# Kernel optimization log

Measured on AMD Instinct MI355X. Metric: run time of the kernel, lower is better.

## Reference

```python
import jax, jax.numpy as jnp
import numpy as np

N_LEVELS = 16
N_FEATS = 2
LOG2_T = 19
BASE_RES = 16.0
FINEST_RES = 512.0
N_POINTS = 1_000_000
HASH_MASK = np.uint32((1 << LOG2_T) - 1)
PRIME1 = np.uint32(2654435761)  # second spatial-hash prime (first is 1)


def setup_inputs() -> dict:
    key = jax.random.key(0)
    k1, k2 = jax.random.split(key)
    x = jax.random.uniform(k1, (N_POINTS, 2), dtype=jnp.float32)
    # nn.init.uniform_(w, -1e-4, 1e-4) per level, stacked: [L, T, F]
    embeddings = (jax.random.uniform(k2, (N_LEVELS, 2 ** LOG2_T, N_FEATS), dtype=jnp.float32) * 2.0 - 1.0) * 1e-4
    return {"x": x, "embeddings": embeddings}


def reference(x, embeddings):
    L = N_LEVELS
    n = x.shape[0]
    # per-level resolutions: floor(base * b**i)
    b = np.exp((np.log(FINEST_RES) - np.log(BASE_RES)) / (L - 1))
    res = np.floor(BASE_RES * b ** np.arange(L)).astype(np.float32)  # [L]
    res_j = jnp.asarray(res)

    pixels = x[None, :, :] * res_j[:, None, None]           # [L, n, 2]
    top_left = jnp.floor(pixels).astype(jnp.int32)          # [L, n, 2]
    offsets = jnp.array([[0, 0], [1, 0], [0, 1], [1, 1]], dtype=jnp.int32)
    box = top_left[:, :, None, :] + offsets[None, None]     # [L, n, 4, 2]
    box = jnp.clip(box, 0, res_j[:, None, None, None].astype(jnp.int32))

    # spatial hash: (c0*1 ^ c1*prime) & mask, with uint32 wraparound like torch int32
    c = box.astype(jnp.uint32)
    addr = ((c[..., 0] * np.uint32(1)) ^ (c[..., 1] * PRIME1)) & HASH_MASK  # [L, n, 4]
    addr = addr.astype(jnp.int32)

    # gather per-level corner features: [L, n, 4, F]
    feats = jax.vmap(lambda table, idx: table[idx])(embeddings, addr)

    # bilinear interpolation
    w = pixels - jnp.floor(pixels)                          # [L, n, 2]
    w0 = w[..., 0:1]
    w1 = w[..., 1:2]
    f0, f1, f2, f3 = feats[:, :, 0], feats[:, :, 1], feats[:, :, 2], feats[:, :, 3]
    f = (f0 * (1 - w0) + f1 * w0) * (1 - w1) + (f2 * (1 - w0) + f3 * w0) * w1  # [L, n, F]

    # concat levels along feature dim -> [n, L*F]
    return jnp.transpose(f, (1, 0, 2)).reshape(n, L * N_FEATS)
```

## Files before the change

### kernel.cpp

```cpp
#include <hip/hip_runtime.h>
#include <cmath>

#define NLVL 16
#define TSIZE (1u << 19)
#define HMASK ((1u << 19) - 1u)
#define PRIME1 2654435761u

struct Params {
    float rf[NLVL];
    int   ri[NLVL];
    int   base[NLVL];
    int   stride[NLVL];
};

__global__ __launch_bounds__(256) void build_dense(
    const float2* __restrict__ emb, float2* __restrict__ dense, Params p)
{
    const int l = blockIdx.y;
    const int cy = blockIdx.x;
    const int ri = p.ri[l];
    if (cy > ri) return;
    const unsigned hy = (unsigned)cy * PRIME1;
    const float2* tab = emb + (size_t)l * TSIZE;
    float2* drow = dense + p.base[l] + (size_t)cy * p.stride[l];
    for (int cx = threadIdx.x; cx <= ri; cx += 256)
        drow[cx] = tab[((unsigned)cx ^ hy) & HMASK];
}

__global__ __launch_bounds__(256) void hash_embed_dense(
    const float2* __restrict__ x,
    const float2* __restrict__ dense,
    float* __restrict__ out,
    Params p, int n)
{
    __shared__ float2 lds[NLVL * 256];
    const int tid = threadIdx.x;
    const int i = blockIdx.x * 256 + tid;
    float2 xy = make_float2(0.f, 0.f);
    if (i < n) xy = x[i];

    #pragma unroll
    for (int half = 0; half < 2; ++half) {
        float4 r0[8], r1[8];
        float w0v[8], w1v[8];
        int edge[8];
        #pragma unroll
        for (int j = 0; j < 8; ++j) {
            const int l = half * 8 + j;
            const float rf = p.rf[l];
            const int ri = p.ri[l];
            const float px = xy.x * rf, py = xy.y * rf;
            const float fx = floorf(px), fy = floorf(py);
            w0v[j] = px - fx;
            w1v[j] = py - fy;
            const int tx = (int)fx, ty = (int)fy;
            const int cx0 = min(tx, ri);
            const int cy0 = min(ty, ri);
            const int cy1 = min(ty + 1, ri);
            edge[j] = (cx0 == ri);
            const float2* tab = dense + p.base[l];
            const float2* a0 = tab + cy0 * p.stride[l] + cx0;
            const float2* a1 = tab + cy1 * p.stride[l] + cx0;
            __builtin_memcpy(&r0[j], a0, 16);
            __builtin_memcpy(&r1[j], a1, 16);
        }
        #pragma unroll
        for (int j = 0; j < 8; ++j) {
            const int l = half * 8 + j;
            const float w0 = w0v[j], w1 = w1v[j];
            const float u0 = 1.f - w0, u1 = 1.f - w1;
            const float e00x = r0[j].x, e00y = r0[j].y;
            const float e01x = edge[j] ? r0[j].x : r0[j].z;
            const float e01y = edge[j] ? r0[j].y : r0[j].w;
            const float e10x = r1[j].x, e10y = r1[j].y;
            const float e11x = edge[j] ? r1[j].x : r1[j].z;
            const float e11y = edge[j] ? r1[j].y : r1[j].w;
            const float g0 = (e00x*u0 + e01x*w0)*u1 + (e10x*u0 + e11x*w0)*w1;
            const float g1 = (e00y*u0 + e01y*w0)*u1 + (e10y*u0 + e11y*w0)*w1;
            lds[l * 256 + tid] = make_float2(g0, g1);
        }
    }
    __syncthreads();

    const float* lf = (const float*)lds;
    const long long total = (long long)n * 32;
    const long long base = (long long)blockIdx.x * 8192;
    #pragma unroll
    for (int it = 0; it < 8; ++it) {
        const int k = (it * 256 + tid) * 4;
        if (base + k < total) {
            const int p2 = k >> 5;
            const int l0 = (k & 31) >> 1;
            float4 v;
            v.x = lf[(l0 * 256 + p2) * 2 + 0];
            v.y = lf[(l0 * 256 + p2) * 2 + 1];
            v.z = lf[((l0 + 1) * 256 + p2) * 2 + 0];
            v.w = lf[((l0 + 1) * 256 + p2) * 2 + 1];
            *(float4*)(out + base + k) = v;
        }
    }
}

__global__ __launch_bounds__(256) void hash_embed_direct(
    const float2* __restrict__ x,
    const float2* __restrict__ emb,
    float* __restrict__ out,
    Params p, int n)
{
    __shared__ float2 lds[NLVL * 256];
    const int tid = threadIdx.x;
    const int i = blockIdx.x * 256 + tid;
    float2 xy = make_float2(0.f, 0.f);
    if (i < n) xy = x[i];

    #pragma unroll
    for (int half = 0; half < 2; ++half) {
        float2 f[32];
        float w0v[8], w1v[8];
        #pragma unroll
        for (int j = 0; j < 8; ++j) {
            const int l = half * 8 + j;
            const float rf = p.rf[l];
            const int ri = p.ri[l];
            const float px = xy.x * rf, py = xy.y * rf;
            const float fx = floorf(px), fy = floorf(py);
            w0v[j] = px - fx;
            w1v[j] = py - fy;
            const int tx = (int)fx, ty = (int)fy;
            const unsigned cx0 = (unsigned)min(tx, ri);
            const unsigned cy0 = (unsigned)min(ty, ri);
            const unsigned cx1 = (unsigned)min(tx + 1, ri);
            const unsigned cy1 = (unsigned)min(ty + 1, ri);
            const unsigned hy0 = cy0 * PRIME1;
            const unsigned hy1 = cy1 * PRIME1;
            const float2* tab = emb + (size_t)l * TSIZE;
            f[j*4+0] = tab[(cx0 ^ hy0) & HMASK];
            f[j*4+1] = tab[(cx1 ^ hy0) & HMASK];
            f[j*4+2] = tab[(cx0 ^ hy1) & HMASK];
            f[j*4+3] = tab[(cx1 ^ hy1) & HMASK];
        }
        #pragma unroll
        for (int j = 0; j < 8; ++j) {
            const int l = half * 8 + j;
            const float w0 = w0v[j], w1 = w1v[j];
            const float u0 = 1.f - w0, u1 = 1.f - w1;
            const float2 f0 = f[j*4+0], f1 = f[j*4+1], f2 = f[j*4+2], f3 = f[j*4+3];
            const float g0 = (f0.x*u0 + f1.x*w0)*u1 + (f2.x*u0 + f3.x*w0)*w1;
            const float g1 = (f0.y*u0 + f1.y*w0)*u1 + (f2.y*u0 + f3.y*w0)*w1;
            lds[l * 256 + tid] = make_float2(g0, g1);
        }
    }
    __syncthreads();

    const float* lf = (const float*)lds;
    const long long total = (long long)n * 32;
    const long long base = (long long)blockIdx.x * 8192;
    #pragma unroll
    for (int it = 0; it < 8; ++it) {
        const int k = (it * 256 + tid) * 4;
        if (base + k < total) {
            const int p2 = k >> 5;
            const int l0 = (k & 31) >> 1;
            float4 v;
            v.x = lf[(l0 * 256 + p2) * 2 + 0];
            v.y = lf[(l0 * 256 + p2) * 2 + 1];
            v.z = lf[((l0 + 1) * 256 + p2) * 2 + 0];
            v.w = lf[((l0 + 1) * 256 + p2) * 2 + 1];
            *(float4*)(out + base + k) = v;
        }
    }
}

extern "C" void kernel_launch(void* const* d_in, const int* in_sizes, int n_in,
                              void* d_out, int out_size, void* d_ws, size_t ws_size,
                              hipStream_t stream) {
    const float2* x = (const float2*)d_in[0];
    const float2* emb = (const float2*)d_in[1];
    float* out = (float*)d_out;
    const int n = in_sizes[0] / 2;

    Params p;
    int off = 0;
    const double b = std::exp((std::log(512.0) - std::log(16.0)) / 15.0);
    for (int l = 0; l < NLVL; ++l) {
        const double r = std::floor(16.0 * std::pow(b, (double)l));
        p.rf[l] = (float)r;
        p.ri[l] = (int)r;
        p.stride[l] = p.ri[l] + 2;
        p.base[l] = off;
        off += (p.ri[l] + 1) * (p.ri[l] + 2);
    }
    const size_t need = (size_t)off * sizeof(float2);

    const int grid = (n + 255) / 256;
    if (ws_size >= need) {
        build_dense<<<dim3(513, 16), 256, 0, stream>>>(emb, (float2*)d_ws, p);
        hash_embed_dense<<<grid, 256, 0, stream>>>(x, (const float2*)d_ws, out, p, n);
    } else {
        hash_embed_direct<<<grid, 256, 0, stream>>>(x, emb, out, p, n);
    }
}
```

Measured before the change: 282.4 us.

## Store dense grid as fp16 corner pairs and write outputs directly without LDS

The dense table builder now stores each cell as an fp16 pair of the cell and its right neighbour (8 bytes), which halves the footprint of the precomputed table and removes the edge select at lookup time. The main kernel loads two 8-byte entries per level and writes each point's 32 floats straight to global memory as float4 stores, dropping the LDS transpose and the barrier. Rounding embeddings to fp16 adds error relative to the fp32 reference, though values near 1e-4 stay within half's normal range. Per-thread 128-byte strided stores may coalesce less well than the old block-contiguous writes.

```diff
diff --git a/kernel.cpp b/kernel.cpp
--- a/kernel.cpp
+++ b/kernel.cpp
@@ -1,4 +1,5 @@
 #include <hip/hip_runtime.h>
+#include <hip/hip_fp16.h>
 #include <cmath>
 
 #define NLVL 16
@@ -13,8 +14,16 @@
     int   stride[NLVL];
 };
 
+__device__ __forceinline__ unsigned pack_h2(float a, float b) {
+    __half2 h = __floats2half2_rn(a, b);
+    unsigned u; __builtin_memcpy(&u, &h, 4); return u;
+}
+__device__ __forceinline__ float2 unpack_h2(unsigned u) {
+    __half2 h; __builtin_memcpy(&h, &u, 4); return __half22float2(h);
+}
+
 __global__ __launch_bounds__(256) void build_dense(
-    const float2* __restrict__ emb, float2* __restrict__ dense, Params p)
+    const float2* __restrict__ emb, uint2* __restrict__ dense, Params p)
 {
     const int l = blockIdx.y;
     const int cy = blockIdx.x;
@@ -22,28 +31,30 @@
     if (cy > ri) return;
     const unsigned hy = (unsigned)cy * PRIME1;
     const float2* tab = emb + (size_t)l * TSIZE;
-    float2* drow = dense + p.base[l] + (size_t)cy * p.stride[l];
-    for (int cx = threadIdx.x; cx <= ri; cx += 256)
-        drow[cx] = tab[((unsigned)cx ^ hy) & HMASK];
+    uint2* drow = dense + p.base[l] + (size_t)cy * p.stride[l];
+    for (int cx = threadIdx.x; cx <= ri; cx += 256) {
+        const float2 e0 = tab[((unsigned)cx ^ hy) & HMASK];
+        const unsigned cx1 = (unsigned)min(cx + 1, ri);
+        const float2 e1 = tab[(cx1 ^ hy) & HMASK];
+        drow[cx] = make_uint2(pack_h2(e0.x, e0.y), pack_h2(e1.x, e1.y));
+    }
 }
 
 __global__ __launch_bounds__(256) void hash_embed_dense(
     const float2* __restrict__ x,
-    const float2* __restrict__ dense,
-    float* __restrict__ out,
+    const uint2* __restrict__ dense,
+    float4* __restrict__ out,
     Params p, int n)
 {
-    __shared__ float2 lds[NLVL * 256];
-    const int tid = threadIdx.x;
-    const int i = blockIdx.x * 256 + tid;
-    float2 xy = make_float2(0.f, 0.f);
-    if (i < n) xy = x[i];
+    const int i = blockIdx.x * 256 + threadIdx.x;
+    if (i >= n) return;
+    const float2 xy = x[i];
+    float4* outp = out + (size_t)i * 8;
 
     #pragma unroll
     for (int half = 0; half < 2; ++half) {
-        float4 r0[8], r1[8];
+        uint2 r0[8], r1[8];
         float w0v[8], w1v[8];
-        int edge[8];
         #pragma unroll
         for (int j = 0; j < 8; ++j) {
             const int l = half * 8 + j;
@@ -57,46 +68,30 @@
             const int cx0 = min(tx, ri);
             const int cy0 = min(ty, ri);
             const int cy1 = min(ty + 1, ri);
-            edge[j] = (cx0 == ri);
-            const float2* tab = dense + p.base[l];
-            const float2* a0 = tab + cy0 * p.stride[l] + cx0;
-            const float2* a1 = tab + cy1 * p.stride[l] + cx0;
-            __builtin_memcpy(&r0[j], a0, 16);
-            __builtin_memcpy(&r1[j], a1, 16);
+            const uint2* tab = dense + p.base[l];
+            r0[j] = tab[cy0 * p.stride[l] + cx0];
+            r1[j] = tab[cy1 * p.stride[l] + cx0];
         }
         #pragma unroll
-        for (int j = 0; j < 8; ++j) {
-            const int l = half * 8 + j;
-            const float w0 = w0v[j], w1 = w1v[j];
-            const float u0 = 1.f - w0, u1 = 1.f - w1;
-            const float e00x = r0[j].x, e00y = r0[j].y;
-            const float e01x = edge[j] ? r0[j].x : r0[j].z;
-            const float e01y = edge[j] ? r0[j].y : r0[j].w;
-            const float e10x = r1[j].x, e10y = r1[j].y;
-            const float e11x = edge[j] ? r1[j].x : r1[j].z;
-            const float e11y = edge[j] ? r1[j].y : r1[j].w;
-            const float g0 = (e00x*u0 + e01x*w0)*u1 + (e10x*u0 + e11x*w0)*w1;
-            const float g1 = (e00y*u0 + e01y*w0)*u1 + (e10y*u0 + e11y*w0)*w1;
-            lds[l * 256 + tid] = make_float2(g0, g1);
-        }
-    }
-    __syncthreads();
-
-    const float* lf = (const float*)lds;
-    const long long total = (long long)n * 32;
-    const long long base = (long long)blockIdx.x * 8192;
-    #pragma unroll
-    for (int it = 0; it < 8; ++it) {
-        const int k = (it * 256 + tid) * 4;
-        if (base + k < total) {
-            const int p2 = k >> 5;
-            const int l0 = (k & 31) >> 1;
+        for (int j = 0; j < 8; j += 2) {
             float4 v;
-            v.x = lf[(l0 * 256 + p2) * 2 + 0];
-            v.y = lf[(l0 * 256 + p2) * 2 + 1];
-            v.z = lf[((l0 + 1) * 256 + p2) * 2 + 0];
-            v.w = lf[((l0 + 1) * 256 + p2) * 2 + 1];
-            *(float4*)(out + base + k) = v;
+            {
+                const float w0 = w0v[j], w1 = w1v[j];
+                const float u0 = 1.f - w0, u1 = 1.f - w1;
+                const float2 e00 = unpack_h2(r0[j].x), e01 = unpack_h2(r0[j].y);
+                const float2 e10 = unpack_h2(r1[j].x), e11 = unpack_h2(r1[j].y);
+                v.x = (e00.x*u0 + e01.x*w0)*u1 + (e10.x*u0 + e11.x*w0)*w1;
+                v.y = (e00.y*u0 + e01.y*w0)*u1 + (e10.y*u0 + e11.y*w0)*w1;
+            }
+            {
+                const float w0 = w0v[j+1], w1 = w1v[j+1];
+                const float u0 = 1.f - w0, u1 = 1.f - w1;
+                const float2 e00 = unpack_h2(r0[j+1].x), e01 = unpack_h2(r0[j+1].y);
+                const float2 e10 = unpack_h2(r1[j+1].x), e11 = unpack_h2(r1[j+1].y);
+                v.z = (e00.x*u0 + e01.x*w0)*u1 + (e10.x*u0 + e11.x*w0)*w1;
+                v.w = (e00.y*u0 + e01.y*w0)*u1 + (e10.y*u0 + e11.y*w0)*w1;
+            }
+            outp[half * 4 + j / 2] = v;
         }
     }
 }
@@ -107,12 +102,9 @@
     float* __restrict__ out,
     Params p, int n)
 {
-    __shared__ float2 lds[NLVL * 256];
-    const int tid = threadIdx.x;
-    const int i = blockIdx.x * 256 + tid;
-    float2 xy = make_float2(0.f, 0.f);
-    if (i < n) xy = x[i];
-
+    const int i = blockIdx.x * 256 + threadIdx.x;
+    if (i >= n) return;
+    const float2 xy = x[i];
     #pragma unroll
     for (int half = 0; half < 2; ++half) {
         float2 f[32];
@@ -124,15 +116,13 @@
             const int ri = p.ri[l];
             const float px = xy.x * rf, py = xy.y * rf;
             const float fx = floorf(px), fy = floorf(py);
-            w0v[j] = px - fx;
-            w1v[j] = py - fy;
+            w0v[j] = px - fx; w1v[j] = py - fy;
             const int tx = (int)fx, ty = (int)fy;
             const unsigned cx0 = (unsigned)min(tx, ri);
             const unsigned cy0 = (unsigned)min(ty, ri);
             const unsigned cx1 = (unsigned)min(tx + 1, ri);
             const unsigned cy1 = (unsigned)min(ty + 1, ri);
-            const unsigned hy0 = cy0 * PRIME1;
-            const unsigned hy1 = cy1 * PRIME1;
+            const unsigned hy0 = cy0 * PRIME1, hy1 = cy1 * PRIME1;
             const float2* tab = emb + (size_t)l * TSIZE;
             f[j*4+0] = tab[(cx0 ^ hy0) & HMASK];
             f[j*4+1] = tab[(cx1 ^ hy0) & HMASK];
@@ -145,28 +135,8 @@
             const float w0 = w0v[j], w1 = w1v[j];
             const float u0 = 1.f - w0, u1 = 1.f - w1;
             const float2 f0 = f[j*4+0], f1 = f[j*4+1], f2 = f[j*4+2], f3 = f[j*4+3];
-            const float g0 = (f0.x*u0 + f1.x*w0)*u1 + (f2.x*u0 + f3.x*w0)*w1;
-            const float g1 = (f0.y*u0 + f1.y*w0)*u1 + (f2.y*u0 + f3.y*w0)*w1;
-            lds[l * 256 + tid] = make_float2(g0, g1);
-        }
-    }
-    __syncthreads();
-
-    const float* lf = (const float*)lds;
-    const long long total = (long long)n * 32;
-    const long long base = (long long)blockIdx.x * 8192;
-    #pragma unroll
-    for (int it = 0; it < 8; ++it) {
-        const int k = (it * 256 + tid) * 4;
-        if (base + k < total) {
-            const int p2 = k >> 5;
-            const int l0 = (k & 31) >> 1;
-            float4 v;
-            v.x = lf[(l0 * 256 + p2) * 2 + 0];
-            v.y = lf[(l0 * 256 + p2) * 2 + 1];
-            v.z = lf[((l0 + 1) * 256 + p2) * 2 + 0];
-            v.w = lf[((l0 + 1) * 256 + p2) * 2 + 1];
-            *(float4*)(out + base + k) = v;
+            out[(size_t)i*32 + l*2 + 0] = (f0.x*u0 + f1.x*w0)*u1 + (f2.x*u0 + f3.x*w0)*w1;
+            out[(size_t)i*32 + l*2 + 1] = (f0.y*u0 + f1.y*w0)*u1 + (f2.y*u0 + f3.y*w0)*w1;
         }
     }
 }
@@ -176,7 +146,6 @@
                               hipStream_t stream) {
     const float2* x = (const float2*)d_in[0];
     const float2* emb = (const float2*)d_in[1];
-    float* out = (float*)d_out;
     const int n = in_sizes[0] / 2;
 
     Params p;
@@ -186,17 +155,18 @@
         const double r = std::floor(16.0 * std::pow(b, (double)l));
         p.rf[l] = (float)r;
         p.ri[l] = (int)r;
-        p.stride[l] = p.ri[l] + 2;
+        p.stride[l] = p.ri[l] + 1;
         p.base[l] = off;
-        off += (p.ri[l] + 1) * (p.ri[l] + 2);
+        off += (p.ri[l] + 1) * (p.ri[l] + 1);
     }
-    const size_t need = (size_t)off * sizeof(float2);
+    const size_t need = (size_t)off * sizeof(uint2);
 
     const int grid = (n + 255) / 256;
     if (ws_size >= need) {
-        build_dense<<<dim3(513, 16), 256, 0, stream>>>(emb, (float2*)d_ws, p);
-        hash_embed_dense<<<grid, 256, 0, stream>>>(x, (const float2*)d_ws, out, p, n);
+        build_dense<<<dim3(513, 16), 256, 0, stream>>>(emb, (uint2*)d_ws, p);
+        hash_embed_dense<<<grid, 256, 0, stream>>>(x, (const uint2*)d_ws,
+                                                   (float4*)d_out, p, n);
     } else {
-        hash_embed_direct<<<grid, 256, 0, stream>>>(x, emb, out, p, n);
+        hash_embed_direct<<<grid, 256, 0, stream>>>(x, emb, (float*)d_out, p, n);
     }
 }
```

Result: slower. 341.0 us (+20.8%).
